# Kernel optimization log

Measured on AMD Instinct MI355X. Metric: run time of the kernel, lower is better.

The kernel has to match this reference:

```python
import jax, jax.numpy as jnp
import numpy as np
import math

BASE_RES, MAX_RES, NUM_LOD, FEAT_DIM = 16, 256, 8, 2
_growth = math.exp((math.log(MAX_RES) - math.log(BASE_RES)) / (NUM_LOD - 1))
LODS = [int(BASE_RES * _growth ** L) for L in range(NUM_LOD)]
N_PTS = 4_000_000


def setup_inputs() -> dict:
    key = jax.random.key(0)
    keys = jax.random.split(key, NUM_LOD + 1)
    inp = {"pts": jax.random.uniform(keys[0], (N_PTS, 2), dtype=jnp.float32)}
    for i, res in enumerate(LODS):
        inp[f"cb{i}"] = jax.random.normal(keys[i + 1], (res * res, FEAT_DIM), dtype=jnp.float32) * 0.01
    return inp


def _forward(pts, codebooks):
    feats = []
    for res, cb in zip(LODS, codebooks):
        # 'closest' interpolation: floor to nearest lower grid cell, row-major index
        xy = jnp.floor(pts * (res - 1)).astype(jnp.int32)  # [N, 2]
        idx = xy[:, 0] + xy[:, 1] * res                    # [N]
        feats.append(cb[idx])                              # [N, feat_dim]
    # torch: cat of unsqueeze(-1) -> [N, feat_dim, num_lod], then reshape
    all_features = jnp.stack(feats, axis=-1)               # [N, feat_dim, num_lod]
    return all_features.reshape(-1, NUM_LOD * FEAT_DIM)


def reference(pts, cb0, cb1, cb2, cb3, cb4, cb5, cb6, cb7):
    return _forward(pts, (cb0, cb1, cb2, cb3, cb4, cb5, cb6, cb7))
```

## Files before the change

### kernel.cpp

```cpp
#include <hip/hip_runtime.h>
#include <math.h>

#define NUM_LOD 8

struct GridParams {
    const float* cb[NUM_LOD];
    int res[NUM_LOD];
};

__global__ __launch_bounds__(256) void densegrid_kernel(
    const float2* __restrict__ pts, GridParams p, float* __restrict__ out, int n)
{
    int i = blockIdx.x * blockDim.x + threadIdx.x;
    if (i >= n) return;

    const float2 pt = pts[i];

    float o[2 * NUM_LOD];
#pragma unroll
    for (int L = 0; L < NUM_LOD; ++L) {
        const int   res = p.res[L];
        const float s   = (float)(res - 1);
        const int ix = (int)floorf(pt.x * s);
        const int iy = (int)floorf(pt.y * s);
        const float2 f = ((const float2*)p.cb[L])[ix + iy * res];
        o[L]           = f.x;
        o[NUM_LOD + L] = f.y;
    }

    float4* o4 = (float4*)(out + (size_t)i * (2 * NUM_LOD));
    o4[0] = make_float4(o[0],  o[1],  o[2],  o[3]);
    o4[1] = make_float4(o[4],  o[5],  o[6],  o[7]);
    o4[2] = make_float4(o[8],  o[9],  o[10], o[11]);
    o4[3] = make_float4(o[12], o[13], o[14], o[15]);
}

extern "C" void kernel_launch(void* const* d_in, const int* in_sizes, int n_in,
                              void* d_out, int out_size, void* d_ws, size_t ws_size,
                              hipStream_t stream)
{
    const float2* pts = (const float2*)d_in[0];
    const int n = in_sizes[0] / 2;

    GridParams p;
    for (int L = 0; L < NUM_LOD; ++L) {
        p.cb[L] = (const float*)d_in[L + 1];
        const int cells = in_sizes[L + 1] / 2;
        p.res[L] = (int)(sqrt((double)cells) + 0.5);
    }

    const int block = 256;
    const int grid  = (n + block - 1) / block;
    densegrid_kernel<<<grid, block, 0, stream>>>(pts, p, (float*)d_out, n);
}
```

Before: 390.7 us.

## Stage small codebooks in LDS and coalesce output writes via shared transpose

The three smallest codebooks are copied into shared memory at the start of every block, so their gathers are served from LDS instead of global or cache memory. Per-thread outputs are staged in a padded shared buffer, and the block then writes them back as contiguous float4 stores, avoiding strided 64-byte-per-thread writes. The block size is raised to 512. The cost is a per-block preload of about 16KB of codebook data, two barriers, and roughly 51KB of LDS per block, which limits occupancy.

```diff
diff --git a/kernel.cpp b/kernel.cpp
--- a/kernel.cpp
+++ b/kernel.cpp
@@ -2,37 +2,70 @@
 #include <math.h>
 
 #define NUM_LOD 8
+#define NLDS 3
+#define BLOCK 512
+#define TPAD 17
 
 struct GridParams {
     const float* cb[NUM_LOD];
     int res[NUM_LOD];
+    int ldsOff[NLDS];
+    int ldsCnt[NLDS];
 };
 
-__global__ __launch_bounds__(256) void densegrid_kernel(
-    const float2* __restrict__ pts, GridParams p, float* __restrict__ out, int n)
+__global__ __launch_bounds__(BLOCK) void densegrid_kernel(
+    const float2* __restrict__ pts, GridParams p, float4* __restrict__ out4, long long n)
 {
-    int i = blockIdx.x * blockDim.x + threadIdx.x;
-    if (i >= n) return;
+    __shared__ float cbLds[4096];
+    __shared__ float tbuf[BLOCK * TPAD];
 
-    const float2 pt = pts[i];
+    const int t = threadIdx.x;
 
-    float o[2 * NUM_LOD];
+    for (int L = 0; L < NLDS; ++L) {
+        const float2* src = (const float2*)p.cb[L];
+        float2* dst = (float2*)&cbLds[p.ldsOff[L]];
+        const int cnt2 = p.ldsCnt[L] >> 1;
+        for (int j = t; j < cnt2; j += BLOCK) dst[j] = src[j];
+    }
+    __syncthreads();
+
+    const long long i = (long long)blockIdx.x * BLOCK + t;
+    if (i < n) {
+        const float2 pt = pts[i];
+        float o[16];
 #pragma unroll
-    for (int L = 0; L < NUM_LOD; ++L) {
-        const int   res = p.res[L];
-        const float s   = (float)(res - 1);
-        const int ix = (int)floorf(pt.x * s);
-        const int iy = (int)floorf(pt.y * s);
-        const float2 f = ((const float2*)p.cb[L])[ix + iy * res];
-        o[L]           = f.x;
-        o[NUM_LOD + L] = f.y;
+        for (int L = 0; L < NUM_LOD; ++L) {
+            const int   res = p.res[L];
+            const float s   = (float)(res - 1);
+            const int ix = (int)floorf(pt.x * s);
+            const int iy = (int)floorf(pt.y * s);
+            const int idx = ix + iy * res;
+            float2 f;
+            if (L < NLDS) {
+                f = ((const float2*)&cbLds[p.ldsOff[L]])[idx];
+            } else {
+                f = ((const float2*)p.cb[L])[idx];
+            }
+            o[L]     = f.x;
+            o[8 + L] = f.y;
+        }
+#pragma unroll
+        for (int j = 0; j < 16; ++j) tbuf[t * TPAD + j] = o[j];
     }
+    __syncthreads();
 
-    float4* o4 = (float4*)(out + (size_t)i * (2 * NUM_LOD));
-    o4[0] = make_float4(o[0],  o[1],  o[2],  o[3]);
-    o4[1] = make_float4(o[4],  o[5],  o[6],  o[7]);
-    o4[2] = make_float4(o[8],  o[9],  o[10], o[11]);
-    o4[3] = make_float4(o[12], o[13], o[14], o[15]);
+    const long long base4 = (long long)blockIdx.x * (BLOCK * 4);
+    const long long lim4  = n * 4;
+#pragma unroll
+    for (int k = 0; k < 4; ++k) {
+        const int m = k * BLOCK + t;
+        const long long g = base4 + m;
+        if (g < lim4) {
+            const int pnt = m >> 2, q = m & 3;
+            const float* src = &tbuf[pnt * TPAD + q * 4];
+            out4[g] = make_float4(src[0], src[1], src[2], src[3]);
+        }
+    }
 }
 
 extern "C" void kernel_launch(void* const* d_in, const int* in_sizes, int n_in,
@@ -40,16 +73,21 @@
                               hipStream_t stream)
 {
     const float2* pts = (const float2*)d_in[0];
-    const int n = in_sizes[0] / 2;
+    const long long n = in_sizes[0] / 2;
 
     GridParams p;
+    int off = 0;
     for (int L = 0; L < NUM_LOD; ++L) {
         p.cb[L] = (const float*)d_in[L + 1];
         const int cells = in_sizes[L + 1] / 2;
         p.res[L] = (int)(sqrt((double)cells) + 0.5);
+        if (L < NLDS) {
+            p.ldsOff[L] = off;
+            p.ldsCnt[L] = in_sizes[L + 1];
+            off += in_sizes[L + 1];
+        }
     }
 
-    const int block = 256;
-    const int grid  = (n + block - 1) / block;
-    densegrid_kernel<<<grid, block, 0, stream>>>(pts, p, (float*)d_out, n);
+    const long long grid = (n + BLOCK - 1) / BLOCK;
+    densegrid_kernel<<<(int)grid, BLOCK, 0, stream>>>(pts, p, (float4*)d_out, n);
 }
```

New measurement: 351.3 us. 1.11x faster.
